# Optimization experiments

Hardware: AMD Instinct MI355X
Metric: run time of the kernel (lower is better)

## Reference

```python
import jax, jax.numpy as jnp
import numpy as np

K_RATIO = 0.01
SIM_THRESHOLD = 0.6


def _gcn_update(feats, W_gcn, b_gcn):
    # feats: [N, C]. Build edges: inverse_similarity < (1 - thr)/2  <=>  cos sim > thr.
    nf = feats / jnp.maximum(jnp.linalg.norm(feats, axis=1, keepdims=True), 1e-12)
    sim = nf @ nf.T                                  # [N, N]
    inv_sim = (1.0 - sim) * 0.5
    adj = (inv_sim < (1.0 - SIM_THRESHOLD) * 0.5).astype(feats.dtype)  # includes self loops
    deg = jnp.sum(adj, axis=1)
    dinv = jax.lax.rsqrt(jnp.maximum(deg, 1.0))      # D^{-1/2}
    agg = dinv[:, None] * (adj @ (dinv[:, None] * feats))
    return agg @ W_gcn + b_gcn                        # [N, C]


def setup_inputs() -> dict:
    key = jax.random.key(0)
    k1, k2, k3 = jax.random.split(key, 3)
    B, C, H, W = 16, 128, 160, 160
    z = jax.random.normal(k1, (B, C, H, W), dtype=jnp.float32)
    score = jax.random.uniform(k2, (B, H, W), dtype=jnp.float32)
    W_gcn = jax.random.normal(k3, (C, C), dtype=jnp.float32) * (1.0 / np.sqrt(C))
    b_gcn = jnp.zeros((C,), dtype=jnp.float32)
    return {"z": z, "score": score, "W_gcn": W_gcn, "b_gcn": b_gcn}


def reference(z, score, W_gcn, b_gcn):
    B, C, H, W = z.shape
    num_select = int(H * W * K_RATIO)                # 256, static
    flat_score = score.reshape(B, H * W)
    _, top_idx = jax.lax.top_k(flat_score, num_select)   # [B, S]

    flat_z = z.reshape(B, C, H * W)
    idx_bcs = jnp.broadcast_to(top_idx[:, None, :], (B, C, num_select))
    top_features = jnp.take_along_axis(flat_z, idx_bcs, axis=2)  # [B, C, S]
    feats = top_features.transpose(0, 2, 1).reshape(B * num_select, C)  # [N, C]

    updated = _gcn_update(feats, W_gcn, b_gcn)        # [N, C]
    updated = updated.reshape(B, num_select, C).transpose(0, 2, 1)  # [B, C, S]

    b_ix = jnp.arange(B)[:, None, None]
    c_ix = jnp.arange(C)[None, :, None]
    new_flat = flat_z.at[b_ix, c_ix, top_idx[:, None, :]].set(updated)
    return new_flat.reshape(B, C, H, W)
```

## Files before the change

### kernel.cpp

```cpp
#include <hip/hip_runtime.h>
#include <hip/hip_bf16.h>

#define HWs 25600
#define NB 16
#define NC 128
#define NS 256
#define NN 4096
#define N4 13107200

#define K1_CPB 1024
#define K1_U 12
#define K2_CPB 2560
#define K2_U 8
#define K3_CPB 2048
#define K3_U 9
#define K2_BASE 3145728
#define K3_BASE 8388608

typedef __attribute__((ext_vector_type(8))) short bf16x8;
typedef __attribute__((ext_vector_type(4))) float f32x4;
typedef __attribute__((ext_vector_type(4))) int i32x4;
typedef unsigned long long u64;

template <int U>
__device__ __forceinline__ void copy_slice(const float4* __restrict__ zz,
                                           float4* __restrict__ oo,
                                           size_t base, int cb, int tid) {
  size_t start = base + (size_t)cb * (U * 256) + tid;
  float4 v[U];
  #pragma unroll
  for (int k = 0; k < U; ++k) v[k] = zz[start + k * 256];
  __builtin_amdgcn_sched_barrier(0);
  #pragma unroll
  for (int k = 0; k < U; ++k) oo[start + k * 256] = v[k];
}

__global__ __launch_bounds__(256) void k1_kernel(const float* __restrict__ z,
                                                 const float* __restrict__ score,
                                                 float* __restrict__ out,
                                                 int* __restrict__ sel) {
  __shared__ unsigned int vals[HWs];
  __shared__ int hist[256];
  __shared__ int scan_s[256];
  __shared__ int scan_eq[256];
  __shared__ int bc_dig, bc_k;
  const int tid = threadIdx.x;
  const int bid = blockIdx.x;

  if (bid >= NB) {
    copy_slice<K1_U>((const float4*)z, (float4*)out, 0, bid - NB, tid);
    return;
  }

  int b = bid;
  const float* sc = score + (size_t)b * HWs;
  for (int i = tid; i < HWs; i += 256) vals[i] = __float_as_uint(sc[i]);
  __syncthreads();

  unsigned prefix = 0; int k = NS;
  for (int d = 3; d >= 0; --d) {
    int sh = d * 8;
    hist[tid] = 0; __syncthreads();
    unsigned maskHigh = (d == 3) ? 0u : (0xFFFFFFFFu << (sh + 8));
    for (int i = tid; i < HWs; i += 256) {
      unsigned v = vals[i];
      if ((v & maskHigh) == prefix) atomicAdd(&hist[(v >> sh) & 255], 1);
    }
    __syncthreads();
    int val = hist[255 - tid];
    scan_s[tid] = val; __syncthreads();
    for (int off = 1; off < 256; off <<= 1) {
      int a = (tid >= off) ? scan_s[tid - off] : 0;
      __syncthreads();
      scan_s[tid] += a; __syncthreads();
    }
    int q = 255 - tid;
    int Sq = scan_s[tid];
    int before = Sq - hist[q];
    if (before < k && k <= Sq) { bc_dig = q; bc_k = k - before; }
    __syncthreads();
    prefix |= ((unsigned)bc_dig) << sh;
    k = bc_k;
    __syncthreads();
  }
  unsigned t = prefix;

  int cstart = tid * 100, cend = cstart + 100;
  int cgt = 0, ceq = 0;
  for (int i = cstart; i < cend; ++i) {
    unsigned v = vals[i];
    cgt += (v > t) ? 1 : 0;
    ceq += (v == t) ? 1 : 0;
  }
  scan_s[tid] = cgt; scan_eq[tid] = ceq; __syncthreads();
  for (int off = 1; off < 256; off <<= 1) {
    int ag = (tid >= off) ? scan_s[tid - off] : 0;
    int ae = (tid >= off) ? scan_eq[tid - off] : 0;
    __syncthreads();
    scan_s[tid] += ag; scan_eq[tid] += ae; __syncthreads();
  }
  int total_gt = scan_s[255];
  int need = NS - total_gt;
  int g = scan_s[tid] - cgt;
  int e = scan_eq[tid] - ceq;
  for (int i = cstart; i < cend; ++i) {
    unsigned v = vals[i];
    if (v > t) { sel[b * NS + g] = i; ++g; }
    else if (v == t) { if (e < need) sel[b * NS + total_gt + e] = i; ++e; }
  }
}

__global__ __launch_bounds__(256) void k2_kernel(const float* __restrict__ z,
                                                 const int* __restrict__ sel,
                                                 float* __restrict__ out,
                                                 float* __restrict__ feats,
                                                 ushort* __restrict__ nfb) {
  const int tid = threadIdx.x;
  const int bid = blockIdx.x;
  if (bid >= NN / 4) {
    copy_slice<K2_U>((const float4*)z, (float4*)out, K2_BASE, bid - NN / 4, tid);
    return;
  }
  int row = bid * 4 + (tid >> 6);
  int lane = tid & 63;
  int b = row >> 8;
  int idx = sel[row];
  const float* zb = z + (size_t)b * NC * HWs + idx;
  float v0 = zb[(size_t)lane * HWs];
  float v1 = zb[(size_t)(lane + 64) * HWs];
  float ss = v0 * v0 + v1 * v1;
  #pragma unroll
  for (int off = 32; off; off >>= 1) ss += __shfl_xor(ss, off);
  float denom = fmaxf(sqrtf(ss), 1e-12f);
  feats[row * NC + lane] = v0;
  feats[row * NC + lane + 64] = v1;
  __hip_bfloat16 h0 = __float2bfloat16(v0 / denom);
  __hip_bfloat16 h1 = __float2bfloat16(v1 / denom);
  nfb[row * NC + lane] = *reinterpret_cast<ushort*>(&h0);
  nfb[row * NC + lane + 64] = *reinterpret_cast<ushort*>(&h1);
}

__global__ __launch_bounds__(256) void k3_kernel(const ushort* __restrict__ nfb,
                                                 const float* __restrict__ z,
                                                 float* __restrict__ out,
                                                 u64* __restrict__ adj) {
  __shared__ __align__(16) ushort tA[64 * 128];
  __shared__ __align__(16) ushort tB[64 * 128];
  __shared__ u64 rowbits[64];
  const int tid = threadIdx.x;
  const int bid = blockIdx.x;
  if (bid >= 4096) {
    copy_slice<K3_U>((const float4*)z, (float4*)out, K3_BASE, bid - 4096, tid);
    return;
  }
  int I0 = (bid & 63) * 64, J0 = (bid >> 6) * 64;
  if (tid < 64) rowbits[tid] = 0ull;
  for (int f = tid; f < 1024; f += 256) {
    int r = f >> 4, c = f & 15;
    int scnk = c ^ (r & 7);
    *(i32x4*)&tA[r * 128 + scnk * 8] = *(const i32x4*)(nfb + (size_t)(I0 + r) * NC + c * 8);
    *(i32x4*)&tB[r * 128 + scnk * 8] = *(const i32x4*)(nfb + (size_t)(J0 + r) * NC + c * 8);
  }
  __syncthreads();
  int w = tid >> 6, l = tid & 63;
  int r = l & 15, kg = l >> 4;
  f32x4 acc[4] = {{0.f, 0.f, 0.f, 0.f}, {0.f, 0.f, 0.f, 0.f},
                  {0.f, 0.f, 0.f, 0.f}, {0.f, 0.f, 0.f, 0.f}};
  int Ar = 16 * w + r;
  #pragma unroll
  for (int kk = 0; kk < 4; ++kk) {
    int chunkA = (kk * 4 + kg) ^ (Ar & 7);
    bf16x8 a = *(bf16x8*)&tA[Ar * 128 + chunkA * 8];
    #pragma unroll
    for (int j = 0; j < 4; ++j) {
      int Bc = 16 * j + r;
      int chunkB = (kk * 4 + kg) ^ (Bc & 7);
      bf16x8 bf = *(bf16x8*)&tB[Bc * 128 + chunkB * 8];
      acc[j] = __builtin_amdgcn_mfma_f32_16x16x32_bf16(a, bf, acc[j], 0, 0, 0);
    }
  }
  #pragma unroll
  for (int q = 0; q < 4; ++q) {
    u64 m = 0ull;
    #pragma unroll
    for (int j = 0; j < 4; ++j) {
      float simv = acc[j][q];
      if ((1.0f - simv) * 0.5f < 0.2f) m |= 1ull << (16 * j + (l & 15));
    }
    if (m) atomicOr(&rowbits[16 * w + (l >> 4) * 4 + q], m);
  }
  __syncthreads();
  if (tid < 64) adj[(size_t)(I0 + tid) * 64 + (bid >> 6)] = rowbits[tid];
}

__global__ __launch_bounds__(256) void k4_kernel(const u64* __restrict__ adj,
                                                 const float* __restrict__ feats,
                                                 const float* __restrict__ Wg,
                                                 const float* __restrict__ bg,
                                                 const int* __restrict__ sel,
                                                 float* __restrict__ out) {
  __shared__ __align__(16) float Wt[NC * 132];
  __shared__ __align__(16) float aggT[16 * 132];
  int tid = threadIdx.x;
  int r0 = blockIdx.x * 16;
  for (int f = tid; f < NC * NC; f += 256) {
    int c = f >> 7, cp = f & 127;
    Wt[cp * 132 + c] = Wg[f];
  }
  int w = tid >> 6, lane = tid & 63;
  for (int rr = 0; rr < 4; ++rr) {
    int lrow = w * 4 + rr;
    int row = r0 + lrow;
    u64 mw = adj[(size_t)row * 64 + lane];
    int ctot = __popcll(mw);
    #pragma unroll
    for (int off = 32; off; off >>= 1) ctot += __shfl_xor(ctot, off);
    float dinv_i = 1.0f / sqrtf(fmaxf((float)ctot, 1.0f));
    float acc0 = 0.f, acc1 = 0.f;
    for (int wi = 0; wi < 64; ++wi) {
      u64 w64 = __shfl((long long)mw, wi);
      while (w64) {
        int bit = __builtin_ctzll(w64);
        w64 &= w64 - 1;
        int j = wi * 64 + bit;
        u64 jm = adj[(size_t)j * 64 + lane];
        int cj = __popcll(jm);
        #pragma unroll
        for (int off = 32; off; off >>= 1) cj += __shfl_xor(cj, off);
        float dj = 1.0f / sqrtf(fmaxf((float)cj, 1.0f));
        acc0 += dj * feats[(size_t)j * NC + lane];
        acc1 += dj * feats[(size_t)j * NC + lane + 64];
      }
    }
    aggT[lrow * 132 + lane] = dinv_i * acc0;
    aggT[lrow * 132 + lane + 64] = dinv_i * acc1;
  }
  __syncthreads();
  int cp = tid & 127;
  int rsub = tid >> 7;
  float acc[8];
  float bb = bg[cp];
  #pragma unroll
  for (int q = 0; q < 8; ++q) acc[q] = bb;
  for (int c4 = 0; c4 < 32; ++c4) {
    float4 w4 = *(const float4*)&Wt[cp * 132 + c4 * 4];
    #pragma unroll
    for (int q = 0; q < 8; ++q) {
      float4 a4 = *(const float4*)&aggT[(rsub + 2 * q) * 132 + c4 * 4];
      acc[q] += a4.x * w4.x + a4.y * w4.y + a4.z * w4.z + a4.w * w4.w;
    }
  }
  #pragma unroll
  for (int q = 0; q < 8; ++q) {
    int row = r0 + rsub + 2 * q;
    int batch = row >> 8;
    int idx = sel[row];
    out[(size_t)(batch * NC + cp) * HWs + idx] = acc[q];
  }
}

extern "C" void kernel_launch(void* const* d_in, const int* in_sizes, int n_in,
                              void* d_out, int out_size, void* d_ws, size_t ws_size,
                              hipStream_t stream) {
  const float* z     = (const float*)d_in[0];
  const float* score = (const float*)d_in[1];
  const float* Wg    = (const float*)d_in[2];
  const float* bg    = (const float*)d_in[3];
  float* out = (float*)d_out;

  char* ws = (char*)d_ws;
  size_t off = 0;
  auto alloc = [&](size_t bytes) {
    void* p = ws + off;
    off = (off + bytes + 255) & ~(size_t)255;
    return p;
  };
  int* sel     = (int*)alloc(NN * sizeof(int));
  float* feats = (float*)alloc((size_t)NN * NC * sizeof(float));
  ushort* nfb  = (ushort*)alloc((size_t)NN * NC * sizeof(ushort));
  u64* adj     = (u64*)alloc((size_t)NN * 64 * sizeof(u64));

  k1_kernel<<<NB + K1_CPB, 256, 0, stream>>>(z, score, out, sel);
  k2_kernel<<<NN / 4 + K2_CPB, 256, 0, stream>>>(z, sel, out, feats, nfb);
  k3_kernel<<<4096 + K3_CPB, 256, 0, stream>>>(nfb, z, out, adj);
  k4_kernel<<<256, 256, 0, stream>>>(adj, feats, Wg, bg, sel, out);
}
```

Measured before the change: 180.4 us.

## Drop 100KB LDS score buffer in top-k kernel and rebalance copy split

Removes the 100KB shared-memory staging of scores in the top-k block, so each radix pass and the selection pass re-read scores straight from global/L2 as float4 vectors. This frees LDS so the copy blocks that share the kernel can run at much higher occupancy. The z-to-out copy is also redistributed: K1 now copies far more chunks while K2 and K3 copy fewer, all with a uniform unroll of 8. The cost is re-reading the score data six times from cache instead of LDS.

```diff
diff --git a/kernel.cpp b/kernel.cpp
--- a/kernel.cpp
+++ b/kernel.cpp
@@ -8,14 +8,12 @@
 #define NN 4096
 #define N4 13107200
 
-#define K1_CPB 1024
-#define K1_U 12
-#define K2_CPB 2560
-#define K2_U 8
-#define K3_CPB 2048
-#define K3_U 9
-#define K2_BASE 3145728
-#define K3_BASE 8388608
+#define K1_CPB 2880
+#define K2_CPB 2240
+#define K3_CPB 1280
+#define CP_U 8
+#define K2_BASE 5898240
+#define K3_BASE 10485760
 
 typedef __attribute__((ext_vector_type(8))) short bf16x8;
 typedef __attribute__((ext_vector_type(4))) float f32x4;
@@ -39,7 +37,6 @@
                                                  const float* __restrict__ score,
                                                  float* __restrict__ out,
                                                  int* __restrict__ sel) {
-  __shared__ unsigned int vals[HWs];
   __shared__ int hist[256];
   __shared__ int scan_s[256];
   __shared__ int scan_eq[256];
@@ -48,23 +45,28 @@
   const int bid = blockIdx.x;
 
   if (bid >= NB) {
-    copy_slice<K1_U>((const float4*)z, (float4*)out, 0, bid - NB, tid);
+    copy_slice<CP_U>((const float4*)z, (float4*)out, 0, bid - NB, tid);
     return;
   }
 
   int b = bid;
   const float* sc = score + (size_t)b * HWs;
-  for (int i = tid; i < HWs; i += 256) vals[i] = __float_as_uint(sc[i]);
-  __syncthreads();
+  const float4* sc4 = (const float4*)sc;
 
   unsigned prefix = 0; int k = NS;
   for (int d = 3; d >= 0; --d) {
     int sh = d * 8;
     hist[tid] = 0; __syncthreads();
     unsigned maskHigh = (d == 3) ? 0u : (0xFFFFFFFFu << (sh + 8));
-    for (int i = tid; i < HWs; i += 256) {
-      unsigned v = vals[i];
-      if ((v & maskHigh) == prefix) atomicAdd(&hist[(v >> sh) & 255], 1);
+    #pragma unroll 5
+    for (int i4 = 0; i4 < 25; ++i4) {
+      float4 f = sc4[tid * 25 + i4];
+      const float* fp = (const float*)&f;
+      #pragma unroll
+      for (int c = 0; c < 4; ++c) {
+        unsigned v = __float_as_uint(fp[c]);
+        if ((v & maskHigh) == prefix) atomicAdd(&hist[(v >> sh) & 255], 1);
+      }
     }
     __syncthreads();
     int val = hist[255 - tid];
@@ -85,12 +87,17 @@
   }
   unsigned t = prefix;
 
-  int cstart = tid * 100, cend = cstart + 100;
   int cgt = 0, ceq = 0;
-  for (int i = cstart; i < cend; ++i) {
-    unsigned v = vals[i];
-    cgt += (v > t) ? 1 : 0;
-    ceq += (v == t) ? 1 : 0;
+  #pragma unroll 5
+  for (int i4 = 0; i4 < 25; ++i4) {
+    float4 f = sc4[tid * 25 + i4];
+    const float* fp = (const float*)&f;
+    #pragma unroll
+    for (int c = 0; c < 4; ++c) {
+      unsigned v = __float_as_uint(fp[c]);
+      cgt += (v > t) ? 1 : 0;
+      ceq += (v == t) ? 1 : 0;
+    }
   }
   scan_s[tid] = cgt; scan_eq[tid] = ceq; __syncthreads();
   for (int off = 1; off < 256; off <<= 1) {
@@ -103,10 +110,16 @@
   int need = NS - total_gt;
   int g = scan_s[tid] - cgt;
   int e = scan_eq[tid] - ceq;
-  for (int i = cstart; i < cend; ++i) {
-    unsigned v = vals[i];
-    if (v > t) { sel[b * NS + g] = i; ++g; }
-    else if (v == t) { if (e < need) sel[b * NS + total_gt + e] = i; ++e; }
+  for (int i4 = 0; i4 < 25; ++i4) {
+    float4 f = sc4[tid * 25 + i4];
+    const float* fp = (const float*)&f;
+    #pragma unroll
+    for (int c = 0; c < 4; ++c) {
+      int i = tid * 100 + i4 * 4 + c;
+      unsigned v = __float_as_uint(fp[c]);
+      if (v > t) { sel[b * NS + g] = i; ++g; }
+      else if (v == t) { if (e < need) sel[b * NS + total_gt + e] = i; ++e; }
+    }
   }
 }
 
@@ -118,7 +131,7 @@
   const int tid = threadIdx.x;
   const int bid = blockIdx.x;
   if (bid >= NN / 4) {
-    copy_slice<K2_U>((const float4*)z, (float4*)out, K2_BASE, bid - NN / 4, tid);
+    copy_slice<CP_U>((const float4*)z, (float4*)out, K2_BASE, bid - NN / 4, tid);
     return;
   }
   int row = bid * 4 + (tid >> 6);
@@ -150,7 +163,7 @@
   const int tid = threadIdx.x;
   const int bid = blockIdx.x;
   if (bid >= 4096) {
-    copy_slice<K3_U>((const float4*)z, (float4*)out, K3_BASE, bid - 4096, tid);
+    copy_slice<CP_U>((const float4*)z, (float4*)out, K3_BASE, bid - 4096, tid);
     return;
   }
   int I0 = (bid & 63) * 64, J0 = (bid >> 6) * 64;
```

Measured after the change: 178.1 us. No clear change (-1.3%).
